# Kernel optimization log

Measured on AMD Instinct MI355X. Metric: run time of the kernel, lower is better.

The kernel has to match this reference:

```python
import jax, jax.numpy as jnp
import numpy as np
from jax import lax

G = 1000  # hard-coded grid size in ConvCNP.forward
LOG_2PI = float(np.log(2.0 * np.pi))


def _conv1d(x, w, b):
    # x: (B, Cin, L), w: (Cout, Cin, K), SAME padding, stride 1 (k=5, pad=2)
    y = lax.conv_general_dilated(x, w, (1,), 'SAME',
                                 dimension_numbers=('NCH', 'OIH', 'NCH'))
    return y + b[None, :, None]


def setup_inputs() -> dict:
    key = jax.random.key(0)
    ks = jax.random.split(key, 16)
    B, Nc, Nt = 32, 2048, 2048
    inp = {
        'x_context': jax.random.normal(ks[0], (B, 1, Nc), jnp.float32),
        'y_context': jax.random.normal(ks[1], (B, 1, Nc), jnp.float32),
        'x_target': jax.random.normal(ks[2], (B, 1, Nt), jnp.float32),
        'y_target': jax.random.normal(ks[3], (B, 1, Nt), jnp.float32),
        # learned kernel lengthscales (nn.Parameter init 0.5)
        'ls_x': jnp.asarray(0.5, jnp.float32),
        'ls_rho': jnp.asarray(0.5, jnp.float32),
        # SimpleCNN(2, 1): channels [2, 16, 32, 16, 2], k=5
        'W1': 0.1 * jax.random.normal(ks[4], (16, 2, 5), jnp.float32),
        'b1': jnp.zeros((16,), jnp.float32),
        'W2': 0.1 * jax.random.normal(ks[5], (32, 16, 5), jnp.float32),
        'b2': jnp.zeros((32,), jnp.float32),
        'W3': 0.1 * jax.random.normal(ks[6], (16, 32, 5), jnp.float32),
        'b3': jnp.zeros((16,), jnp.float32),
        'W4': 0.1 * jax.random.normal(ks[7], (2, 16, 5), jnp.float32),
        'b4': jnp.zeros((2,), jnp.float32),
    }
    return inp


def _forward(x_context, y_context, x_target, y_target,
             ls_x, ls_rho, W1, b1, W2, b2, W3, b3, W4, b4):
    B = x_context.shape[0]
    xc = x_context[:, 0, :]            # (B, Nc)
    xt = x_target[:, 0, :]             # (B, Nt)
    t = jnp.linspace(-2.2, 2.2, G).astype(x_context.dtype)  # (G,)

    # phi(y) = [1, y] density/signal channels: (B, 2, Nc)
    phi = jnp.concatenate([jnp.ones_like(y_context), y_context], axis=1)

    # EQ-kernel interpolation context -> grid: w[b,g,n] = exp(-(t_g-x_n)^2/(2 l^2))
    d2 = (t[None, :, None] - xc[:, None, :]) ** 2           # (B, G, Nc)
    w_x = jnp.exp(-d2 / (2.0 * ls_x * ls_x))
    h = jnp.einsum('bgn,bcn->bcg', w_x, phi)                # (B, 2, G)

    density = h[:, 0:1, :]
    rest = h[:, 1:, :] / (density + 1e-8)
    h = jnp.concatenate([density, rest], axis=1)            # (B, 2, G)

    # SimpleCNN
    y = jax.nn.relu(_conv1d(h, W1, b1))
    y = jax.nn.relu(_conv1d(y, W2, b2))
    y = jax.nn.relu(_conv1d(y, W3, b3))
    y = _conv1d(y, W4, b4)                                  # (B, 2, G)
    y_mu_grid = y[:, 0:1, :]
    y_sigma_grid = jax.nn.softplus(y[:, 1:2, :])
    y_grid = jnp.concatenate([y_mu_grid, y_sigma_grid], axis=1)  # (B, 2, G)

    # EQ-kernel interpolation grid -> targets
    d2t = (xt[:, :, None] - t[None, None, :]) ** 2          # (B, Nt, G)
    w_rho = jnp.exp(-d2t / (2.0 * ls_rho * ls_rho))
    y_pred = jnp.einsum('btg,bcg->bct', w_rho, y_grid)      # (B, 2, Nt)

    mu = y_pred[:, 0:1, :]
    sigma = y_pred[:, 1:2, :]

    # Normal(mu, sigma).log_prob(y_target), mean over points, sum over batch
    z = (y_target - mu) / sigma
    logp = -0.5 * z * z - jnp.log(sigma) - 0.5 * LOG_2PI    # (B, 1, Nt)
    loss = -jnp.sum(jnp.mean(logp, axis=-1))
    return mu.transpose(0, 2, 1), sigma.transpose(0, 2, 1), loss


def reference(x_context, y_context, x_target, y_target,
              ls_x, ls_rho, W1, b1, W2, b2, W3, b3, W4, b4):
    return _forward(x_context, y_context, x_target, y_target,
                    ls_x, ls_rho, W1, b1, W2, b2, W3, b3, W4, b4)
```

## Files before the change

kernel.cpp:

```cpp
#include <hip/hip_runtime.h>
#include <math.h>

#define G     1000
#define B     32
#define NC    2048
#define NT    2048
#define BN    (B * NT)
#define LOG2E 1.4426950408889634f
#define LN2PI 1.8378770664093453f

#if __has_builtin(__builtin_amdgcn_exp2f)
#define EXP2F(x) __builtin_amdgcn_exp2f(x)
#else
#define EXP2F(x) exp2f(x)
#endif

__global__ __launch_bounds__(512) void k_smooth(
    const float* __restrict__ xc, const float* __restrict__ yc,
    const float* __restrict__ ls_x, float* __restrict__ h,
    float* __restrict__ loss_slot) {
  __shared__ float2 sxy[NC];
  __shared__ float2 part[8][128];
  if (blockIdx.x == 0 && blockIdx.y == 0 && threadIdx.x == 0) *loss_slot = 0.f;

  int tid = threadIdx.x;
  int b = blockIdx.y, tile = blockIdx.x;
  float ls  = ls_x[0];
  float s   = sqrtf(0.5f * LOG2E) / ls;
  float dlt = s * (4.4f / 999.f);

  const float* xb = xc + b * NC;
  const float* yb = yc + b * NC;
  for (int n = tid; n < NC; n += 512) sxy[n] = make_float2(s * xb[n], yb[n]);
  __syncthreads();

  int lane = tid & 63, w = tid >> 6;
  int ns = lane & 7, gr = lane >> 3;
  int g0 = tile * 128 + gr * 16;
  float v0 = s * -2.2f + dlt * (float)g0;
  float r  = EXP2F(-2.f * dlt * dlt);

  float h0[16], h1[16];
  #pragma unroll
  for (int j = 0; j < 16; ++j) { h0[j] = 0.f; h1[j] = 0.f; }

  const float2* base = sxy + w * 256 + ns;
  #pragma unroll 4
  for (int i = 0; i < 32; ++i) {
    float2 v = base[i * 8];
    float a = v.x - v0;
    float W = EXP2F(64.f - a * a);
    float q = EXP2F(fmaf(2.f * dlt, a, -dlt * dlt));
    #pragma unroll
    for (int j = 0; j < 16; ++j) {
      h0[j] += W;
      h1[j] = fmaf(W, v.y, h1[j]);
      W *= q; q *= r;
    }
  }
  #pragma unroll
  for (int m = 1; m < 8; m <<= 1) {
    #pragma unroll
    for (int j = 0; j < 16; ++j) {
      h0[j] += __shfl_xor(h0[j], m);
      h1[j] += __shfl_xor(h1[j], m);
    }
  }
  {
    int j0 = ns * 2;
    part[w][gr * 16 + j0]     = make_float2(h0[j0], h1[j0]);
    part[w][gr * 16 + j0 + 1] = make_float2(h0[j0 + 1], h1[j0 + 1]);
  }
  __syncthreads();

  if (tid < 128) {
    int g = tile * 128 + tid;
    if (g < G) {
      float d0 = 0.f, d1 = 0.f;
      #pragma unroll
      for (int k = 0; k < 8; ++k) { float2 pv = part[k][tid]; d0 += pv.x; d1 += pv.y; }
      d0 *= 0x1p-64f;
      d1 *= 0x1p-64f;
      h[(b * 2 + 0) * G + g] = d0;
      h[(b * 2 + 1) * G + g] = d1 / (d0 + 1e-8f);
    }
  }
}

#define TILE  48
#define NTILE 21
#define CSTR  68

template <int CIN, int COUT, int S4>
__device__ __forceinline__ void conv8(
    const float* __restrict__ in, float* __restrict__ out,
    const float4* __restrict__ wf4, const float* __restrict__ w4p,
    const float* __restrict__ bias, int tid) {
  if (tid < COUT * 8) {
    int oc = tid % COUT;
    int i0 = (tid / COUT) * 8;
    float acc[8];
    float bb = bias[oc];
    #pragma unroll
    for (int p = 0; p < 8; ++p) acc[p] = bb;
    for (int ic = 0; ic < CIN; ++ic) {
      const float4* ip = (const float4*)(in + ic * CSTR + i0);
      float4 A = ip[0], Bv = ip[1], C = ip[2];
      float v[12] = {A.x, A.y, A.z, A.w, Bv.x, Bv.y, Bv.z, Bv.w, C.x, C.y, C.z, C.w};
      float4 w = wf4[oc * S4 + ic];
      float w4v = w4p[ic * COUT + oc];
      #pragma unroll
      for (int p = 0; p < 8; ++p)
        acc[p] = fmaf(v[p], w.x, fmaf(v[p+1], w.y, fmaf(v[p+2], w.z,
                 fmaf(v[p+3], w.w, fmaf(v[p+4], w4v, acc[p])))));
    }
    float* op = out + oc * CSTR + i0 + 2;
    #pragma unroll
    for (int j = 0; j < 4; ++j)
      *(float2*)(op + 2 * j) = make_float2(fmaxf(acc[2*j], 0.f), fmaxf(acc[2*j+1], 0.f));
  }
}

__global__ __launch_bounds__(256, 2) void k_conv(
    const float* __restrict__ h,
    const float* __restrict__ W1, const float* __restrict__ Bs1,
    const float* __restrict__ W2, const float* __restrict__ Bs2,
    const float* __restrict__ W3, const float* __restrict__ Bs3,
    const float* __restrict__ W4, const float* __restrict__ Bs4,
    float* __restrict__ yg) {
  __shared__ __align__(16) float bufA[32 * CSTR], bufB[32 * CSTR];
  __shared__ float4 wf1[16 * 3], wf2[32 * 17], wf3[16 * 33];
  __shared__ float  w41[2 * 16], w42[16 * 32], w43[32 * 16];
  __shared__ float  wt4[162];
  __shared__ float  sB1[16], sB2[32], sB3[16], sB4[2];

  int tid  = threadIdx.x;
  int tile = blockIdx.x, b = blockIdx.y;
  int ts   = tile * TILE;

  if (tid < 32) {
    int oc = tid >> 1, ic = tid & 1, a = oc * 10 + ic * 5;
    wf1[oc * 3 + ic] = make_float4(W1[a], W1[a+1], W1[a+2], W1[a+3]);
    w41[ic * 16 + oc] = W1[a + 4];
  }
  for (int pr = tid; pr < 512; pr += 256) {
    int oc = pr >> 4, ic = pr & 15, a = oc * 80 + ic * 5;
    wf2[oc * 17 + ic] = make_float4(W2[a], W2[a+1], W2[a+2], W2[a+3]);
    w42[ic * 32 + oc] = W2[a + 4];
  }
  for (int pr = tid; pr < 512; pr += 256) {
    int oc = pr >> 5, ic = pr & 31, a = oc * 160 + ic * 5;
    wf3[oc * 33 + ic] = make_float4(W3[a], W3[a+1], W3[a+2], W3[a+3]);
    w43[ic * 16 + oc] = W3[a + 4];
  }
  for (int i = tid; i < 160; i += 256) wt4[(i / 80) * 81 + i % 80] = W4[i];
  if (tid < 16)       sB1[tid]      = Bs1[tid];
  else if (tid < 48)  sB2[tid - 16] = Bs2[tid - 16];
  else if (tid < 64)  sB3[tid - 48] = Bs3[tid - 48];
  else if (tid < 66)  sB4[tid - 64] = Bs4[tid - 64];

  for (int i = tid; i < 2 * CSTR; i += 256) {
    int c = i >= CSTR, col = i - c * CSTR;
    int g = ts + col - 10;
    bufA[c * CSTR + col] = (g >= 0 && g < G) ? h[(b * 2 + c) * G + g] : 0.f;
  }
  __syncthreads();

  conv8<2, 16, 3>(bufA, bufB, wf1, w41, sB1, tid);
  __syncthreads();
  conv8<16, 32, 17>(bufB, bufA, wf2, w42, sB2, tid);
  __syncthreads();
  conv8<32, 16, 33>(bufA, bufB, wf3, w43, sB3, tid);
  __syncthreads();

  if (tid < 96) {
    int oc = tid >= 48;
    int j  = tid - oc * 48;
    int i  = 10 + j;
    float sacc = sB4[oc];
    #pragma unroll
    for (int ic = 0; ic < 16; ++ic) {
      const float* ip = bufB + ic * CSTR + i - 2;
      #pragma unroll
      for (int k = 0; k < 5; ++k)
        sacc = fmaf(ip[k], wt4[oc * 81 + ic * 5 + k], sacc);
    }
    int gp = ts + j;
    if (gp < G) {
      if (oc == 0) {
        yg[(b * 2 + 0) * G + gp] = sacc;
      } else {
        float sp_ = fmaxf(sacc, 0.f) + log1pf(__expf(-fabsf(sacc)));
        yg[(b * 2 + 1) * G + gp] = sp_;
      }
    }
  }
}

__global__ __launch_bounds__(512) void k_pred(
    const float* __restrict__ xt, const float* __restrict__ yt,
    const float* __restrict__ ls_rho, const float* __restrict__ yg,
    float* __restrict__ out) {
  __shared__ float4 sp[512];
  __shared__ float pA0[512], pA1[512], pB0[512], pB1[512];
  __shared__ float red[8];

  int tid = threadIdx.x;
  int b = blockIdx.y, tile = blockIdx.x;
  float ls = ls_rho[0];
  float s  = sqrtf(0.5f * LOG2E) / ls;
  float dl = s * (4.4f / 999.f);

  const float* y0 = yg + (b * 2 + 0) * G;
  const float* y1 = yg + (b * 2 + 1) * G;
  {
    int g0 = 2 * tid, g1 = 2 * tid + 1;
    float a0 = (g0 < G) ? y0[g0] : 0.f, b0_ = (g0 < G) ? y1[g0] : 0.f;
    float a1 = (g1 < G) ? y0[g1] : 0.f, b1_ = (g1 < G) ? y1[g1] : 0.f;
    sp[tid] = make_float4(a0, b0_, a1, b1_);
  }
  __syncthreads();

  int lane = tid & 63, wv = tid >> 6;
  int ta = tile * 128 + lane;
  float ua = s * xt[b * NT + ta];
  float ub = s * xt[b * NT + ta + 64];
  float base = 2.2f * s - dl * (float)(wv * 128);
  float aa = ua + base, ab = ub + base;
  float Wa = EXP2F(64.f - aa * aa), qa = EXP2F(dl * (aa + aa) - dl * dl);
  float Wb = EXP2F(64.f - ab * ab), qb = EXP2F(dl * (ab + ab) - dl * dl);
  float r  = EXP2F(-2.f * dl * dl);

  float muA = 0.f, sgA = 0.f, muB = 0.f, sgB = 0.f;
  const float4* p = sp + wv * 64;
  #pragma unroll 4
  for (int i = 0; i < 64; ++i) {
    float4 v = p[i];
    muA = fmaf(Wa, v.x, muA); sgA = fmaf(Wa, v.y, sgA); Wa *= qa; qa *= r;
    muB = fmaf(Wb, v.x, muB); sgB = fmaf(Wb, v.y, sgB); Wb *= qb; qb *= r;
    muA = fmaf(Wa, v.z, muA); sgA = fmaf(Wa, v.w, sgA); Wa *= qa; qa *= r;
    muB = fmaf(Wb, v.z, muB); sgB = fmaf(Wb, v.w, sgB); Wb *= qb; qb *= r;
  }
  pA0[tid] = muA; pA1[tid] = sgA; pB0[tid] = muB; pB1[tid] = sgB;
  __syncthreads();

  float lp = 0.f;
  if (tid < 128) {
    int which = tid >> 6, l = tid & 63;
    int t = tile * 128 + which * 64 + l;
    const float* q0 = which ? pB0 : pA0;
    const float* q1 = which ? pB1 : pA1;
    float mu = 0.f, sg = 0.f;
    #pragma unroll
    for (int k = 0; k < 8; ++k) { mu += q0[l + 64 * k]; sg += q1[l + 64 * k]; }
    mu *= 0x1p-64f;
    sg *= 0x1p-64f;
    out[b * NT + t]      = mu;
    out[BN + b * NT + t] = sg;
    float z = (yt[b * NT + t] - mu) / sg;
    lp = -0.5f * z * z - __logf(sg) - 0.5f * LN2PI;
  }
  #pragma unroll
  for (int m = 32; m; m >>= 1) lp += __shfl_xor(lp, m);
  if ((tid & 63) == 0) red[tid >> 6] = lp;
  __syncthreads();
  if (tid == 0) {
    float tot = 0.f;
    #pragma unroll
    for (int i = 0; i < 8; ++i) tot += red[i];
    atomicAdd(out + 2 * BN, -tot * (1.f / (float)NT));
  }
}

extern "C" void kernel_launch(void* const* d_in, const int* in_sizes, int n_in,
                              void* d_out, int out_size, void* d_ws, size_t ws_size,
                              hipStream_t stream) {
  const float* xc  = (const float*)d_in[0];
  const float* yc  = (const float*)d_in[1];
  const float* xt  = (const float*)d_in[2];
  const float* yt  = (const float*)d_in[3];
  const float* lsx = (const float*)d_in[4];
  const float* lsr = (const float*)d_in[5];
  const float* W1  = (const float*)d_in[6];  const float* b1 = (const float*)d_in[7];
  const float* W2  = (const float*)d_in[8];  const float* b2 = (const float*)d_in[9];
  const float* W3  = (const float*)d_in[10]; const float* b3 = (const float*)d_in[11];
  const float* W4  = (const float*)d_in[12]; const float* b4 = (const float*)d_in[13];

  float* out = (float*)d_out;
  float* h   = (float*)d_ws;
  float* yg  = h + B * 2 * G;

  k_smooth<<<dim3(8, B), 512, 0, stream>>>(xc, yc, lsx, h, out + 2 * BN);
  k_conv<<<dim3(NTILE, B), 256, 0, stream>>>(h, W1, b1, W2, b2, W3, b3, W4, b4, yg);
  k_pred<<<dim3(16, B), 512, 0, stream>>>(xt, yt, lsr, yg, out);
}
```

Baseline: 42.31 us.

## Prepack conv weights in smooth kernel and shrink conv tiles for occupancy

```diff
diff --git a/kernel.cpp b/kernel.cpp
--- a/kernel.cpp
+++ b/kernel.cpp
@@ -15,16 +15,46 @@
 #define EXP2F(x) exp2f(x)
 #endif
 
+#define PW1F4 128000
+#define PW1S  128128
+#define PW2F4 128160
+#define PW2S  130208
+#define PW3F4 130720
+#define PW3S  132768
+#define PW4F4 133280
+#define PW4S  133408
+
 __global__ __launch_bounds__(512) void k_smooth(
     const float* __restrict__ xc, const float* __restrict__ yc,
     const float* __restrict__ ls_x, float* __restrict__ h,
-    float* __restrict__ loss_slot) {
+    float* __restrict__ loss_slot,
+    const float* __restrict__ W1, const float* __restrict__ W2,
+    const float* __restrict__ W3, const float* __restrict__ W4,
+    float* __restrict__ ws) {
   __shared__ float2 sxy[NC];
   __shared__ float2 part[8][128];
-  if (blockIdx.x == 0 && blockIdx.y == 0 && threadIdx.x == 0) *loss_slot = 0.f;
 
   int tid = threadIdx.x;
   int b = blockIdx.y, tile = blockIdx.x;
+
+  if (tile == 0 && b == 0) {
+    if (tid == 0) *loss_slot = 0.f;
+    float4* p1 = (float4*)(ws + PW1F4); float4* p2 = (float4*)(ws + PW2F4);
+    float4* p3 = (float4*)(ws + PW3F4); float4* p4 = (float4*)(ws + PW4F4);
+    if (tid < 32)  { int oc = tid >> 1, ic = tid & 1,  a = oc * 10 + ic * 5;
+      p1[oc * 2 + ic]  = make_float4(W1[a], W1[a+1], W1[a+2], W1[a+3]);
+      ws[PW1S + ic * 16 + oc] = W1[a + 4]; }
+    for (int i = tid; i < 512; i += 512) { int oc = i >> 4, ic = i & 15, a = oc * 80 + ic * 5;
+      p2[oc * 16 + ic] = make_float4(W2[a], W2[a+1], W2[a+2], W2[a+3]);
+      ws[PW2S + ic * 32 + oc] = W2[a + 4]; }
+    for (int i = tid; i < 512; i += 512) { int oc = i >> 5, ic = i & 31, a = oc * 160 + ic * 5;
+      p3[oc * 32 + ic] = make_float4(W3[a], W3[a+1], W3[a+2], W3[a+3]);
+      ws[PW3S + ic * 16 + oc] = W3[a + 4]; }
+    if (tid < 32)  { int oc = tid >> 4, ic = tid & 15, a = oc * 80 + ic * 5;
+      p4[oc * 16 + ic] = make_float4(W4[a], W4[a+1], W4[a+2], W4[a+3]);
+      ws[PW4S + ic * 2 + oc] = W4[a + 4]; }
+  }
+
   float ls  = ls_x[0];
   float s   = sqrtf(0.5f * LOG2E) / ls;
   float dlt = s * (4.4f / 999.f);
@@ -87,27 +117,28 @@
   }
 }
 
-#define TILE  48
-#define NTILE 21
-#define CSTR  68
-
-template <int CIN, int COUT, int S4>
-__device__ __forceinline__ void conv8(
+#define TILE  32
+#define NTILE 32
+#define CSTR  52
+
+template <int CIN, int COUT, int NSUB>
+__device__ __forceinline__ void conv8g(
     const float* __restrict__ in, float* __restrict__ out,
     const float4* __restrict__ wf4, const float* __restrict__ w4p,
     const float* __restrict__ bias, int tid) {
-  if (tid < COUT * 8) {
+  if (tid < COUT * NSUB) {
     int oc = tid % COUT;
     int i0 = (tid / COUT) * 8;
     float acc[8];
     float bb = bias[oc];
     #pragma unroll
     for (int p = 0; p < 8; ++p) acc[p] = bb;
+    #pragma unroll
     for (int ic = 0; ic < CIN; ++ic) {
       const float4* ip = (const float4*)(in + ic * CSTR + i0);
       float4 A = ip[0], Bv = ip[1], C = ip[2];
       float v[12] = {A.x, A.y, A.z, A.w, Bv.x, Bv.y, Bv.z, Bv.w, C.x, C.y, C.z, C.w};
-      float4 w = wf4[oc * S4 + ic];
+      float4 w = wf4[oc * CIN + ic];
       float w4v = w4p[ic * COUT + oc];
       #pragma unroll
       for (int p = 0; p < 8; ++p)
@@ -121,43 +152,21 @@
   }
 }
 
-__global__ __launch_bounds__(256, 2) void k_conv(
+__global__ __launch_bounds__(256, 4) void k_conv(
     const float* __restrict__ h,
-    const float* __restrict__ W1, const float* __restrict__ Bs1,
-    const float* __restrict__ W2, const float* __restrict__ Bs2,
-    const float* __restrict__ W3, const float* __restrict__ Bs3,
-    const float* __restrict__ W4, const float* __restrict__ Bs4,
-    float* __restrict__ yg) {
+    const float* __restrict__ Bs1, const float* __restrict__ Bs2,
+    const float* __restrict__ Bs3, const float* __restrict__ Bs4,
+    const float* __restrict__ ws, float* __restrict__ yg) {
   __shared__ __align__(16) float bufA[32 * CSTR], bufB[32 * CSTR];
-  __shared__ float4 wf1[16 * 3], wf2[32 * 17], wf3[16 * 33];
-  __shared__ float  w41[2 * 16], w42[16 * 32], w43[32 * 16];
-  __shared__ float  wt4[162];
-  __shared__ float  sB1[16], sB2[32], sB3[16], sB4[2];
 
   int tid  = threadIdx.x;
   int tile = blockIdx.x, b = blockIdx.y;
   int ts   = tile * TILE;
 
-  if (tid < 32) {
-    int oc = tid >> 1, ic = tid & 1, a = oc * 10 + ic * 5;
-    wf1[oc * 3 + ic] = make_float4(W1[a], W1[a+1], W1[a+2], W1[a+3]);
-    w41[ic * 16 + oc] = W1[a + 4];
-  }
-  for (int pr = tid; pr < 512; pr += 256) {
-    int oc = pr >> 4, ic = pr & 15, a = oc * 80 + ic * 5;
-    wf2[oc * 17 + ic] = make_float4(W2[a], W2[a+1], W2[a+2], W2[a+3]);
-    w42[ic * 32 + oc] = W2[a + 4];
-  }
-  for (int pr = tid; pr < 512; pr += 256) {
-    int oc = pr >> 5, ic = pr & 31, a = oc * 160 + ic * 5;
-    wf3[oc * 33 + ic] = make_float4(W3[a], W3[a+1], W3[a+2], W3[a+3]);
-    w43[ic * 16 + oc] = W3[a + 4];
-  }
-  for (int i = tid; i < 160; i += 256) wt4[(i / 80) * 81 + i % 80] = W4[i];
-  if (tid < 16)       sB1[tid]      = Bs1[tid];
-  else if (tid < 48)  sB2[tid - 16] = Bs2[tid - 16];
-  else if (tid < 64)  sB3[tid - 48] = Bs3[tid - 48];
-  else if (tid < 66)  sB4[tid - 64] = Bs4[tid - 64];
+  const float4* pw1 = (const float4*)(ws + PW1F4);
+  const float4* pw2 = (const float4*)(ws + PW2F4);
+  const float4* pw3 = (const float4*)(ws + PW3F4);
+  const float4* pw4 = (const float4*)(ws + PW4F4);
 
   for (int i = tid; i < 2 * CSTR; i += 256) {
     int c = i >= CSTR, col = i - c * CSTR;
@@ -166,27 +175,28 @@
   }
   __syncthreads();
 
-  conv8<2, 16, 3>(bufA, bufB, wf1, w41, sB1, tid);
-  __syncthreads();
-  conv8<16, 32, 17>(bufB, bufA, wf2, w42, sB2, tid);
-  __syncthreads();
-  conv8<32, 16, 33>(bufA, bufB, wf3, w43, sB3, tid);
-  __syncthreads();
-
-  if (tid < 96) {
-    int oc = tid >= 48;
-    int j  = tid - oc * 48;
+  conv8g<2, 16, 6>(bufA, bufB, pw1, ws + PW1S, Bs1, tid);
+  __syncthreads();
+  conv8g<16, 32, 6>(bufB, bufA, pw2, ws + PW2S, Bs2, tid);
+  __syncthreads();
+  conv8g<32, 16, 6>(bufA, bufB, pw3, ws + PW3S, Bs3, tid);
+  __syncthreads();
+
+  if (tid < 64) {
+    int oc = tid >= 32;
+    int j  = tid - oc * 32;
     int i  = 10 + j;
-    float sacc = sB4[oc];
-    #pragma unroll
-    for (int ic = 0; ic < 16; ++ic) {
-      const float* ip = bufB + ic * CSTR + i - 2;
-      #pragma unroll
-      for (int k = 0; k < 5; ++k)
-        sacc = fmaf(ip[k], wt4[oc * 81 + ic * 5 + k], sacc);
-    }
     int gp = ts + j;
     if (gp < G) {
+      float sacc = Bs4[oc];
+      #pragma unroll
+      for (int ic = 0; ic < 16; ++ic) {
+        const float* ip = bufB + ic * CSTR + i - 2;
+        float4 w = pw4[oc * 16 + ic];
+        float w4v = ws[PW4S + ic * 2 + oc];
+        sacc = fmaf(ip[0], w.x, fmaf(ip[1], w.y, fmaf(ip[2], w.z,
+               fmaf(ip[3], w.w, fmaf(ip[4], w4v, sacc)))));
+      }
       if (oc == 0) {
         yg[(b * 2 + 0) * G + gp] = sacc;
       } else {
@@ -287,10 +297,12 @@
   const float* W4  = (const float*)d_in[12]; const float* b4 = (const float*)d_in[13];
 
   float* out = (float*)d_out;
-  float* h   = (float*)d_ws;
-  float* yg  = h + B * 2 * G;
-
-  k_smooth<<<dim3(8, B), 512, 0, stream>>>(xc, yc, lsx, h, out + 2 * BN);
-  k_conv<<<dim3(NTILE, B), 256, 0, stream>>>(h, W1, b1, W2, b2, W3, b3, W4, b4, yg);
+  float* ws  = (float*)d_ws;
+  float* h   = ws;
+  float* yg  = ws + B * 2 * G;
+
+  k_smooth<<<dim3(8, B), 512, 0, stream>>>(xc, yc, lsx, h, out + 2 * BN,
+                                           W1, W2, W3, W4, ws);
+  k_conv<<<dim3(NTILE, B), 256, 0, stream>>>(h, b1, b2, b3, b4, ws, yg);
   k_pred<<<dim3(16, B), 512, 0, stream>>>(xt, yt, lsr, yg, out);
 }
```

After: 44.90 us. 6.1% more time.
